# Kernel optimization log

Measured on AMD Instinct MI355X. Metric: run time of the kernel, lower is better.

## Reference

```python
import jax, jax.numpy as jnp
import numpy as np

T, N, G, H, COV, TW, E = 96, 1024, 128, 512, 8, 8, 32768
D2 = TW * (TW - 1)          # 56, GNN summary width
IN = COV + D2               # 64, exogenous input width


def setup_inputs() -> dict:
    key = jax.random.key(0)
    ks = jax.random.split(key, 32)
    s = 1.0 / np.sqrt(H)

    def u(k, shape):
        return jax.random.uniform(k, shape, jnp.float32, -s, s)

    inp = {
        "input": jax.random.normal(ks[0], (T, 1, IN), jnp.float32),
        "x_nodes": jax.random.normal(ks[1], (T, N, N), jnp.float32),
        "edge_index": jax.random.randint(ks[2], (T, 2, E), 0, N, dtype=jnp.int64),
        "W1": u(ks[3], (N, G)), "b1": u(ks[4], (G,)),
        "W2": u(ks[5], (G, G)), "b2": u(ks[6], (G,)),
        "Wfc": u(ks[7], (G * N, D2)), "bfc": u(ks[8], (D2,)),
        "W_ii": u(ks[9], (IN, H)), "W_gi": u(ks[10], (D2, H)), "W_hi": u(ks[11], (H, H)), "b_i": u(ks[12], (H,)),
        "W_if": u(ks[13], (IN, H)), "W_gf": u(ks[14], (D2, H)), "W_hf": u(ks[15], (H, H)), "b_f": u(ks[16], (H,)),
        "W_ig": u(ks[17], (IN, H)), "W_gg": u(ks[18], (D2, H)), "W_hg": u(ks[19], (H, H)), "b_g": u(ks[20], (H,)),
        "W_io": u(ks[21], (IN, H)), "W_go": u(ks[22], (D2, H)), "W_ho": u(ks[23], (H, H)), "b_o": u(ks[24], (H,)),
    }
    return inp


def reference(input, x_nodes, edge_index,
              W1, b1, W2, b2, Wfc, bfc,
              W_ii, W_gi, W_hi, b_i,
              W_if, W_gf, W_hf, b_f,
              W_ig, W_gg, W_hg, b_g,
              W_io, W_go, W_ho, b_o):
    self_loops = jnp.arange(N, dtype=edge_index.dtype)

    def gcn_conv(x, src, dst, dinv, W, b):
        # GCNConv: out[dst] += d^-1/2[src] d^-1/2[dst] * (x @ W)[src], plus bias
        xw = x @ W                                   # [N, F_out]
        norm = dinv[src] * dinv[dst]                 # [E+N]
        msg = xw[src] * norm[:, None]
        return jax.ops.segment_sum(msg, dst, num_segments=N) + b

    def step(carry, inputs):
        h, c = carry
        x_t, xg, ei = inputs                         # [1,IN], [N,N], [2,E]
        src = jnp.concatenate([ei[0], self_loops])   # add self-loops
        dst = jnp.concatenate([ei[1], self_loops])
        deg = jax.ops.segment_sum(jnp.ones(src.shape, jnp.float32), dst, num_segments=N)
        dinv = jnp.where(deg > 0, jax.lax.rsqrt(jnp.maximum(deg, 1.0)), 0.0)

        xh = jax.nn.relu(gcn_conv(xg, src, dst, dinv, W1, b1))
        xh = gcn_conv(xh, src, dst, dinv, W2, b2)    # [N, G]
        g = jax.nn.relu(xh.reshape(1, -1) @ Wfc + bfc)  # [1, D2]

        i = jax.nn.sigmoid(x_t @ W_ii + g @ W_gi + h @ W_hi + b_i)
        f = jax.nn.sigmoid(x_t @ W_if + g @ W_gf + h @ W_hf + b_f)
        gt = jnp.tanh(x_t @ W_ig + g @ W_gg + h @ W_hg + b_g)
        o = jax.nn.sigmoid(x_t @ W_io + g @ W_go + h @ W_ho + b_o)
        c = f * c + i * gt
        h = o * jnp.tanh(c)
        return (h, c), h

    h0 = jnp.zeros((1, H), jnp.float32)
    c0 = jnp.zeros((1, H), jnp.float32)
    (h, c), outputs = jax.lax.scan(step, (h0, c0), (input, x_nodes, edge_index))
    return outputs, h, c
```

## Files before the change

### kernel.cpp

```cpp
#include <hip/hip_runtime.h>
#include <stdint.h>

#define T_    96
#define TC_   32
#define N_    1024
#define G_    128
#define H_    512
#define E_    32768
#define EN_   33792
#define D2_   56
#define IN_   64
#define KFC_  131072

typedef __bf16 bf16_t;
typedef __bf16 bf16x8 __attribute__((ext_vector_type(8)));
typedef float  f32x4  __attribute__((ext_vector_type(4)));
typedef unsigned short u16;
typedef unsigned long long u64;

struct PtrQuadF { const float* p[4]; };

__device__ inline bf16x8 cvt8(const float* p) {
    const f32x4 a0 = *(const f32x4*)p;
    const f32x4 a1 = *(const f32x4*)(p + 4);
    bf16x8 r;
    r[0] = (bf16_t)a0[0]; r[1] = (bf16_t)a0[1]; r[2] = (bf16_t)a0[2]; r[3] = (bf16_t)a0[3];
    r[4] = (bf16_t)a1[0]; r[5] = (bf16_t)a1[1]; r[6] = (bf16_t)a1[2]; r[7] = (bf16_t)a1[3];
    return r;
}


__global__ __launch_bounds__(256) void deg_kernel(const int* __restrict__ ei, int* __restrict__ deg) {
    int t = blockIdx.y;
    int idx = blockIdx.x * 256 + threadIdx.x;
    if (idx >= EN_) return;
    int d = (idx < E_) ? ei[(size_t)t * 2 * E_ + E_ + idx] : (idx - E_);
    atomicAdd(&deg[t * N_ + d], 1);
}

__global__ __launch_bounds__(1024) void scan_kernel(const int* __restrict__ deg, int* __restrict__ rowptr,
                                                    int* __restrict__ fill, float* __restrict__ dinv) {
    int t = blockIdx.x, i = threadIdx.x;
    __shared__ int a[N_], b[N_];
    int d = deg[t * N_ + i];
    a[i] = d;
    __syncthreads();
    int* cur = a; int* nxt = b;
    for (int off = 1; off < N_; off <<= 1) {
        int v = cur[i];
        if (i >= off) v += cur[i - off];
        nxt[i] = v;
        __syncthreads();
        int* tmp = cur; cur = nxt; nxt = tmp;
    }
    int incl = cur[i];
    int start = incl - d + t * EN_;
    rowptr[t * N_ + i] = start;
    fill[t * N_ + i] = start;
    dinv[t * N_ + i] = rsqrtf((float)d);
}

__global__ __launch_bounds__(256) void fill_kernel(const int* __restrict__ ei, int* __restrict__ fill,
                                                   const float* __restrict__ dinv, u64* __restrict__ ecv) {
    int t = blockIdx.y;
    int idx = blockIdx.x * 256 + threadIdx.x;
    if (idx >= EN_) return;
    int s, d;
    if (idx < E_) {
        s = ei[(size_t)t * 2 * E_ + idx];
        d = ei[(size_t)t * 2 * E_ + E_ + idx];
    } else {
        s = d = idx - E_;
    }
    float nrm = dinv[t * N_ + s] * dinv[t * N_ + d];
    int pos = atomicAdd(&fill[t * N_ + d], 1);
    ecv[pos] = ((u64)__float_as_uint(nrm) << 32) | (unsigned int)s;
}


__global__ __launch_bounds__(256) void transpose_kernel(const float* __restrict__ src, bf16_t* __restrict__ dst,
                                                        int R, int C, int Cpad) {
    __shared__ bf16_t tile[64][65];
    int rb = blockIdx.x * 64, cb = blockIdx.y * 64;
    int tx = threadIdx.x & 63, ty = threadIdx.x >> 6;
#pragma unroll
    for (int i = 0; i < 16; i++) {
        int r = rb + ty * 16 + i;
        int c = cb + tx;
        float v = 0.f;
        if (r < R && c < C) v = src[(size_t)r * C + c];
        tile[ty * 16 + i][tx] = (bf16_t)v;
    }
    __syncthreads();
#pragma unroll
    for (int i = 0; i < 16; i++) {
        int c = cb + ty * 16 + i;
        int r = rb + tx;
        if (c < Cpad && r < R) dst[(size_t)c * R + r] = tile[tx][ty * 16 + i];
    }
}


__global__ __launch_bounds__(256) void transpose16_kernel(const bf16_t* __restrict__ src, bf16_t* __restrict__ dst) {
    __shared__ bf16_t tile[64][65];
    int tl = blockIdx.z;
    const bf16_t* s = src + (size_t)tl * 128 * N_;
    bf16_t* d = dst + (size_t)tl * N_ * 128;
    int rb = blockIdx.y * 64, cb = blockIdx.x * 64;
    int tx = threadIdx.x & 63, ty = threadIdx.x >> 6;
#pragma unroll
    for (int i = 0; i < 16; i++)
        tile[ty * 16 + i][tx] = s[(size_t)(rb + ty * 16 + i) * N_ + cb + tx];
    __syncthreads();
#pragma unroll
    for (int i = 0; i < 16; i++)
        d[(size_t)(cb + ty * 16 + i) * 128 + rb + tx] = tile[tx][ty * 16 + i];
}


__global__ __launch_bounds__(256) void whcvt_kernel(PtrQuadF Wh, bf16_t* __restrict__ dst) {
    int g = blockIdx.y;
    int idx = blockIdx.x * 256 + threadIdx.x;
    dst[(size_t)g * H_ * H_ + idx] = (bf16_t)Wh.p[g][idx];
}


template<bool BF32>
__global__ __launch_bounds__(256) void gemm_g(const bf16_t* __restrict__ A, const void* __restrict__ Bp,
                                              bf16_t* __restrict__ C, const float* __restrict__ bias, int relu,
                                              int K, int Mtiles, size_t sA, size_t sB, size_t sC, int ldc) {
    int t = blockIdx.y;
    int mi = blockIdx.x % Mtiles, ni = blockIdx.x / Mtiles;
    int tid = threadIdx.x;
    int w = tid >> 6, l = tid & 63;
    int wm = w & 1, wn = w >> 1;
    int lm = l & 15, lq = l >> 4;
    f32x4 acc[4][4] = {};
    const bf16_t* Ab = A + sA * t + (size_t)(mi * 128 + wm * 64 + lm) * K + lq * 8;
    size_t bO = sB * t + (size_t)(ni * 128 + wn * 64 + lm) * K + lq * 8;
    const bf16_t* Bb16 = (const bf16_t*)Bp + bO;
    const float*  Bb32 = (const float*)Bp + bO;
    for (int k0 = 0; k0 < K; k0 += 32) {
        bf16x8 af[4], bfv[4];
#pragma unroll
        for (int i = 0; i < 4; i++) af[i] = *(const bf16x8*)(Ab + (size_t)i * 16 * K + k0);
#pragma unroll
        for (int i = 0; i < 4; i++) {
            if (BF32) bfv[i] = cvt8(Bb32 + (size_t)i * 16 * K + k0);
            else      bfv[i] = *(const bf16x8*)(Bb16 + (size_t)i * 16 * K + k0);
        }
#pragma unroll
        for (int mt = 0; mt < 4; mt++)
#pragma unroll
            for (int nt = 0; nt < 4; nt++)
                acc[mt][nt] = __builtin_amdgcn_mfma_f32_16x16x32_bf16(af[mt], bfv[nt], acc[mt][nt], 0, 0, 0);
    }
#pragma unroll
    for (int mt = 0; mt < 4; mt++)
#pragma unroll
        for (int nt = 0; nt < 4; nt++) {
            int colg = ni * 128 + wn * 64 + nt * 16 + lm;
            float bv = bias ? bias[colg] : 0.f;
#pragma unroll
            for (int r = 0; r < 4; r++) {
                int row = mi * 128 + wm * 64 + mt * 16 + lq * 4 + r;
                float v = acc[mt][nt][r] + bv;
                if (relu) v = fmaxf(v, 0.f);
                C[sC * t + (size_t)row * ldc + colg] = (bf16_t)v;
            }
        }
}


__device__ inline void spmm_acc(u64 q, const bf16_t* Fb, int l, float& a0, float& a1) {
    int c = (int)(unsigned int)q;
    float wn = __uint_as_float((unsigned int)(q >> 32));
    unsigned int pk = *(const unsigned int*)(Fb + (size_t)c * 128 + 2 * l);
    a0 += wn * __uint_as_float(pk << 16);
    a1 += wn * __uint_as_float(pk & 0xffff0000u);
}

__global__ __launch_bounds__(256) void spmm_kernel(const int* __restrict__ rowptr, const int* __restrict__ deg,
                                                   const u64* __restrict__ ecv, const bf16_t* __restrict__ F,
                                                   const float* __restrict__ bias, int relu,
                                                   bf16_t* __restrict__ out, int t0) {
    int tl = blockIdx.y, t = t0 + tl;
    int w = threadIdx.x >> 6, l = threadIdx.x & 63;
    int r = blockIdx.x * 4 + w;
    int start = rowptr[t * N_ + r];
    int n = deg[t * N_ + r];
    const bf16_t* Fb = F + (size_t)tl * N_ * 128;
    const u64* ep = ecv + start;
    float a0 = 0.f, a1 = 0.f;
    int e = 0;
    for (; e + 4 <= n; e += 4) {
        u64 q0 = ep[e], q1 = ep[e + 1], q2 = ep[e + 2], q3 = ep[e + 3];
        spmm_acc(q0, Fb, l, a0, a1);
        spmm_acc(q1, Fb, l, a0, a1);
        spmm_acc(q2, Fb, l, a0, a1);
        spmm_acc(q3, Fb, l, a0, a1);
    }
    for (; e < n; e++) spmm_acc(ep[e], Fb, l, a0, a1);
    float v0 = a0 + bias[2 * l], v1 = a1 + bias[2 * l + 1];
    if (relu) { v0 = fmaxf(v0, 0.f); v1 = fmaxf(v1, 0.f); }
    bf16_t b0 = (bf16_t)v0, b1 = (bf16_t)v1;
    unsigned int po = (unsigned int)*(u16*)&b0 | ((unsigned int)*(u16*)&b1 << 16);
    *(unsigned int*)((u16*)(out + ((size_t)tl * N_ + r) * 128) + 2 * l) = po;
}


__global__ __launch_bounds__(256) void gfc_kernel(const bf16_t* __restrict__ XH2, const bf16_t* __restrict__ WfcT,
                                                  float* __restrict__ g_acc, int t0) {
    int tid = threadIdx.x;
    int w = tid >> 6, l = tid & 63;
    int lm = l & 15, lq = l >> 4;
    int n = w * 16 + lm;
    size_t k0 = (size_t)blockIdx.x * 1024;
    f32x4 acc[2] = {};
    const bf16_t* Ab = XH2 + (size_t)lm * KFC_ + k0 + lq * 8;
    const bf16_t* Bb = WfcT + (size_t)n * KFC_ + k0 + lq * 8;
    for (int ks = 0; ks < 32; ks++) {
        bf16x8 bfr = *(const bf16x8*)(Bb + ks * 32);
        bf16x8 a0  = *(const bf16x8*)(Ab + ks * 32);
        bf16x8 a1  = *(const bf16x8*)(Ab + (size_t)16 * KFC_ + ks * 32);
        acc[0] = __builtin_amdgcn_mfma_f32_16x16x32_bf16(a0, bfr, acc[0], 0, 0, 0);
        acc[1] = __builtin_amdgcn_mfma_f32_16x16x32_bf16(a1, bfr, acc[1], 0, 0, 0);
    }
#pragma unroll
    for (int mt = 0; mt < 2; mt++)
#pragma unroll
        for (int r = 0; r < 4; r++) {
            int t = t0 + mt * 16 + lq * 4 + r;
            if (n < D2_) atomicAdd(&g_acc[t * 64 + n], acc[mt][r]);
        }
}


__global__ __launch_bounds__(512) void pregate_kernel(const float* __restrict__ xin, const float* __restrict__ g_acc,
                                                      const float* __restrict__ bfc,
                                                      PtrQuadF Wi, PtrQuadF Wg, PtrQuadF Wb,
                                                      float* __restrict__ out) {
    int gate = blockIdx.x, t = blockIdx.y, j = threadIdx.x;
    __shared__ float gl[D2_];
    __shared__ float xl[IN_];
    if (j < D2_) gl[j] = fmaxf(g_acc[t * 64 + j] + bfc[j], 0.f);
    if (j < IN_) xl[j] = xin[t * IN_ + j];
    __syncthreads();
    const float* wi = Wi.p[gate];
    const float* wg = Wg.p[gate];
    float acc = Wb.p[gate][j];
#pragma unroll 4
    for (int k = 0; k < IN_; k++) acc += xl[k] * wi[k * H_ + j];
#pragma unroll 4
    for (int k = 0; k < D2_; k++) acc += gl[k] * wg[k * H_ + j];
    out[(t * 4 + gate) * H_ + j] = acc;
}


__global__ __launch_bounds__(256) void lstm_kernel(const bf16_t* __restrict__ Whb, const float* __restrict__ pregate,
                                                   u64* __restrict__ h_slot, float* __restrict__ out) {
    int tid = threadIdx.x, bid = blockIdx.x;
    int jl = tid >> 3, kc = tid & 7;
    int j = bid * 32 + jl;
    int k0 = kc * 64;

    uint32_t w[128];
#pragma unroll
    for (int g4 = 0; g4 < 4; g4++) {
        const bf16_t* W = Whb + (size_t)g4 * H_ * H_;
#pragma unroll
        for (int m = 0; m < 32; m++) {
            int k = k0 + 2 * m;
            uint32_t lo = *(const u16*)(W + (size_t)k * H_ + j);
            uint32_t hi = *(const u16*)(W + (size_t)(k + 1) * H_ + j);
            w[g4 * 32 + m] = lo | (hi << 16);
        }
    }

    __shared__ __align__(16) float hl[H_];
    hl[tid] = 0.f;
    hl[tid + 256] = 0.f;
    float c = 0.f;
    __syncthreads();

    for (int step = 0; step < 96; step++) {
        float p0 = 0.f, p1 = 0.f, p2 = 0.f, p3 = 0.f;
        if (kc == 0) {
            const float* pre = pregate + (size_t)step * (4 * H_);
            p0 = pre[0 * H_ + j]; p1 = pre[1 * H_ + j];
            p2 = pre[2 * H_ + j]; p3 = pre[3 * H_ + j];
        }

        float s0 = 0.f, s1 = 0.f, s2 = 0.f, s3 = 0.f;
        const float4* h4 = (const float4*)(hl + k0);
#pragma unroll
        for (int q = 0; q < 16; q++) {
            float4 hq = h4[q];
#pragma unroll
            for (int p = 0; p < 2; p++) {
                float h0 = p ? hq.z : hq.x;
                float h1 = p ? hq.w : hq.y;
                int mi = q * 2 + p;
                uint32_t wv;
                wv = w[0 * 32 + mi];
                s0 += __uint_as_float(wv << 16) * h0 + __uint_as_float(wv & 0xffff0000u) * h1;
                wv = w[1 * 32 + mi];
                s1 += __uint_as_float(wv << 16) * h0 + __uint_as_float(wv & 0xffff0000u) * h1;
                wv = w[2 * 32 + mi];
                s2 += __uint_as_float(wv << 16) * h0 + __uint_as_float(wv & 0xffff0000u) * h1;
                wv = w[3 * 32 + mi];
                s3 += __uint_as_float(wv << 16) * h0 + __uint_as_float(wv & 0xffff0000u) * h1;
            }
        }
        s0 += __shfl_xor(s0, 1); s0 += __shfl_xor(s0, 2); s0 += __shfl_xor(s0, 4);
        s1 += __shfl_xor(s1, 1); s1 += __shfl_xor(s1, 2); s1 += __shfl_xor(s1, 4);
        s2 += __shfl_xor(s2, 1); s2 += __shfl_xor(s2, 2); s2 += __shfl_xor(s2, 4);
        s3 += __shfl_xor(s3, 1); s3 += __shfl_xor(s3, 2); s3 += __shfl_xor(s3, 4);

        if (kc == 0) {
            float ig = 1.f / (1.f + __expf(-(s0 + p0)));
            float fg = 1.f / (1.f + __expf(-(s1 + p1)));
            float gg = tanhf(s2 + p2);
            float og = 1.f / (1.f + __expf(-(s3 + p3)));
            c = fg * c + ig * gg;
            float h = og * tanhf(c);
            if (step < 95) {
                u64 v = ((u64)(unsigned int)(step + 1) << 32) | (u64)__float_as_uint(h);
                __hip_atomic_store(&h_slot[(size_t)step * H_ + j], v, __ATOMIC_RELAXED, __HIP_MEMORY_SCOPE_AGENT);
            }
            out[step * H_ + j] = h;
            if (step == 95) {
                out[96 * H_ + j] = h;
                out[97 * H_ + j] = c;
            }
        }
        if (step < 95) {
            __syncthreads();
            if (tid < 64) {
                unsigned int want = (unsigned int)(step + 1);
                const u64* base = h_slot + (size_t)step * H_ + tid * 8;
                u64 v[8];
                int need = 0xff;
                while (need) {
#pragma unroll
                    for (int s = 0; s < 8; s++)
                        if (need & (1 << s))
                            v[s] = __hip_atomic_load(&base[s], __ATOMIC_RELAXED, __HIP_MEMORY_SCOPE_AGENT);
                    int nd = 0;
#pragma unroll
                    for (int s = 0; s < 8; s++)
                        if ((need & (1 << s)) && (unsigned int)(v[s] >> 32) != want) nd |= 1 << s;
                    need = nd;
                    if (need) __builtin_amdgcn_s_sleep(1);
                }
                float4 f0, f1;
                f0.x = __uint_as_float((unsigned int)v[0]); f0.y = __uint_as_float((unsigned int)v[1]);
                f0.z = __uint_as_float((unsigned int)v[2]); f0.w = __uint_as_float((unsigned int)v[3]);
                f1.x = __uint_as_float((unsigned int)v[4]); f1.y = __uint_as_float((unsigned int)v[5]);
                f1.z = __uint_as_float((unsigned int)v[6]); f1.w = __uint_as_float((unsigned int)v[7]);
                ((float4*)hl)[tid * 2] = f0;
                ((float4*)hl)[tid * 2 + 1] = f1;
            }
            __syncthreads();
        }
    }
}


extern "C" void kernel_launch(void* const* d_in, const int* in_sizes, int n_in,
                              void* d_out, int out_size, void* d_ws, size_t ws_size,
                              hipStream_t stream) {
    const float* xin    = (const float*)d_in[0];
    const float* xnodes = (const float*)d_in[1];
    const int*   ei     = (const int*)d_in[2];
    const float* W1  = (const float*)d_in[3];
    const float* b1  = (const float*)d_in[4];
    const float* W2  = (const float*)d_in[5];
    const float* b2  = (const float*)d_in[6];
    const float* Wfc = (const float*)d_in[7];
    const float* bfc = (const float*)d_in[8];

    PtrQuadF Wi = {{(const float*)d_in[9],  (const float*)d_in[13], (const float*)d_in[17], (const float*)d_in[21]}};
    PtrQuadF Wg = {{(const float*)d_in[10], (const float*)d_in[14], (const float*)d_in[18], (const float*)d_in[22]}};
    PtrQuadF Wh = {{(const float*)d_in[11], (const float*)d_in[15], (const float*)d_in[19], (const float*)d_in[23]}};
    PtrQuadF Wb = {{(const float*)d_in[12], (const float*)d_in[16], (const float*)d_in[20], (const float*)d_in[24]}};

    char* ws = (char*)d_ws;
    size_t off = 0;
    auto alloc = [&](size_t bytes) { void* p = ws + off; off += (bytes + 255) & ~(size_t)255; return p; };

    bf16_t* C1T     = (bf16_t*)alloc((size_t)TC_ * 128 * N_ * 2);
    bf16_t* C1      = (bf16_t*)alloc((size_t)TC_ * N_ * 128 * 2);
    bf16_t* XH1     = (bf16_t*)alloc((size_t)TC_ * N_ * 128 * 2);
    bf16_t* C2      = (bf16_t*)alloc((size_t)TC_ * N_ * 128 * 2);
    bf16_t* XH2     = (bf16_t*)alloc((size_t)TC_ * N_ * 128 * 2);
    u64*    ecv     = (u64*)   alloc((size_t)T_ * EN_ * 8);
    int*    deg     = (int*)   alloc((size_t)T_ * N_ * 4);
    int*    rowptr  = (int*)   alloc((size_t)T_ * N_ * 4);
    int*    fillp   = (int*)   alloc((size_t)T_ * N_ * 4);
    float*  dinv    = (float*) alloc((size_t)T_ * N_ * 4);
    bf16_t* W1t     = (bf16_t*)alloc((size_t)128 * 1024 * 2);
    bf16_t* W2t     = (bf16_t*)alloc((size_t)128 * 128 * 2);
    bf16_t* WfcT    = (bf16_t*)alloc((size_t)64 * KFC_ * 2);
    bf16_t* Whb     = (bf16_t*)alloc((size_t)4 * H_ * H_ * 2);
    float*  g_acc   = (float*) alloc((size_t)T_ * 64 * 4);
    float*  pregate = (float*) alloc((size_t)T_ * 4 * H_ * 4);
    u64*    h_slot  = (u64*)   alloc((size_t)T_ * H_ * 8);

    hipMemsetAsync(deg, 0, (size_t)T_ * N_ * 4, stream);
    hipMemsetAsync(g_acc, 0, (size_t)T_ * 64 * 4, stream);

    deg_kernel<<<dim3(132, T_), 256, 0, stream>>>(ei, deg);
    scan_kernel<<<T_, 1024, 0, stream>>>(deg, rowptr, fillp, dinv);
    fill_kernel<<<dim3(132, T_), 256, 0, stream>>>(ei, fillp, dinv, ecv);

    transpose_kernel<<<dim3(16, 2), 256, 0, stream>>>(W1, W1t, 1024, 128, 128);
    transpose_kernel<<<dim3(2, 2), 256, 0, stream>>>(W2, W2t, 128, 128, 128);
    transpose_kernel<<<dim3(2048, 1), 256, 0, stream>>>(Wfc, WfcT, KFC_, D2_, 64);
    whcvt_kernel<<<dim3(1024, 4), 256, 0, stream>>>(Wh, Whb);

    for (int c = 0; c < T_ / TC_; c++) {
        int t0 = c * TC_;
        gemm_g<true><<<dim3(8, TC_), 256, 0, stream>>>(
            W1t, xnodes + (size_t)t0 * N_ * N_, C1T, nullptr, 0,
            1024, 1, 0, (size_t)N_ * N_, (size_t)128 * N_, N_);
        transpose16_kernel<<<dim3(16, 2, TC_), 256, 0, stream>>>(C1T, C1);
        spmm_kernel<<<dim3(256, TC_), 256, 0, stream>>>(rowptr, deg, ecv, C1, b1, 1, XH1, t0);
        gemm_g<false><<<dim3(8, TC_), 256, 0, stream>>>(
            XH1, W2t, C2, nullptr, 0,
            128, 8, (size_t)N_ * 128, 0, (size_t)N_ * 128, 128);
        spmm_kernel<<<dim3(256, TC_), 256, 0, stream>>>(rowptr, deg, ecv, C2, b2, 0, XH2, t0);
        gfc_kernel<<<128, 256, 0, stream>>>(XH2, WfcT, g_acc, t0);
    }

    pregate_kernel<<<dim3(4, T_), 512, 0, stream>>>(xin, g_acc, bfc, Wi, Wg, Wb, pregate);

    lstm_kernel<<<16, 256, 0, stream>>>(Whb, pregate, h_slot, (float*)d_out);
}
```

Baseline: 1.587 ms.

## Fuse CSR build into one kernel, drop C1 transpose, enlarge time chunk

The degree, scan and fill kernels become one per-timestep block that does its degree counting and fill atomics in shared memory, which removes two launches, the memset and the global atomics. The first GCN GEMM now takes x_nodes as the fp32 A operand and writes C1 directly in node-major layout, so the intermediate transpose kernel and its buffer go away. The time chunk grows from 32 to 48 steps, and gfc handles three 16-row M tiles instead of two. In exchange, a single block per timestep builds the CSR serially over all edges, which limits parallelism, and the larger chunk needs bigger workspace buffers.

```diff
diff --git a/kernel.cpp b/kernel.cpp
--- a/kernel.cpp
+++ b/kernel.cpp
@@ -2,7 +2,7 @@
 #include <stdint.h>
 
 #define T_    96
-#define TC_   32
+#define TC_   48
 #define N_    1024
 #define G_    128
 #define H_    512
@@ -30,51 +30,45 @@
 }
 
 
-__global__ __launch_bounds__(256) void deg_kernel(const int* __restrict__ ei, int* __restrict__ deg) {
-    int t = blockIdx.y;
-    int idx = blockIdx.x * 256 + threadIdx.x;
-    if (idx >= EN_) return;
-    int d = (idx < E_) ? ei[(size_t)t * 2 * E_ + E_ + idx] : (idx - E_);
-    atomicAdd(&deg[t * N_ + d], 1);
-}
-
-__global__ __launch_bounds__(1024) void scan_kernel(const int* __restrict__ deg, int* __restrict__ rowptr,
-                                                    int* __restrict__ fill, float* __restrict__ dinv) {
-    int t = blockIdx.x, i = threadIdx.x;
-    __shared__ int a[N_], b[N_];
-    int d = deg[t * N_ + i];
-    a[i] = d;
-    __syncthreads();
-    int* cur = a; int* nxt = b;
+__global__ __launch_bounds__(1024) void build_kernel(const int* __restrict__ ei,
+                                                     int* __restrict__ rowptr_g, int* __restrict__ deg_g,
+                                                     u64* __restrict__ ecv) {
+    int t = blockIdx.x, tid = threadIdx.x;
+    __shared__ int sdeg[N_];
+    __shared__ int sa[N_], sb[N_];
+    __shared__ int sfill[N_];
+    __shared__ float sdinv[N_];
+    sdeg[tid] = 0;
+    __syncthreads();
+    const int* src_p = ei + (size_t)t * 2 * E_;
+    const int* dst_p = src_p + E_;
+    for (int e = tid; e < E_; e += 1024) atomicAdd(&sdeg[dst_p[e]], 1);
+    __syncthreads();
+    int d = sdeg[tid] + 1;
+    sa[tid] = d;
+    __syncthreads();
+    int* cur = sa; int* nxt = sb;
     for (int off = 1; off < N_; off <<= 1) {
-        int v = cur[i];
-        if (i >= off) v += cur[i - off];
-        nxt[i] = v;
+        int v = cur[tid];
+        if (tid >= off) v += cur[tid - off];
+        nxt[tid] = v;
         __syncthreads();
         int* tmp = cur; cur = nxt; nxt = tmp;
     }
-    int incl = cur[i];
-    int start = incl - d + t * EN_;
-    rowptr[t * N_ + i] = start;
-    fill[t * N_ + i] = start;
-    dinv[t * N_ + i] = rsqrtf((float)d);
-}
-
-__global__ __launch_bounds__(256) void fill_kernel(const int* __restrict__ ei, int* __restrict__ fill,
-                                                   const float* __restrict__ dinv, u64* __restrict__ ecv) {
-    int t = blockIdx.y;
-    int idx = blockIdx.x * 256 + threadIdx.x;
-    if (idx >= EN_) return;
-    int s, d;
-    if (idx < E_) {
-        s = ei[(size_t)t * 2 * E_ + idx];
-        d = ei[(size_t)t * 2 * E_ + E_ + idx];
-    } else {
-        s = d = idx - E_;
-    }
-    float nrm = dinv[t * N_ + s] * dinv[t * N_ + d];
-    int pos = atomicAdd(&fill[t * N_ + d], 1);
-    ecv[pos] = ((u64)__float_as_uint(nrm) << 32) | (unsigned int)s;
+    int start = cur[tid] - d + t * EN_;
+    rowptr_g[t * N_ + tid] = start;
+    deg_g[t * N_ + tid] = d;
+    sfill[tid] = start;
+    sdinv[tid] = rsqrtf((float)d);
+    __syncthreads();
+    for (int e = tid; e < EN_; e += 1024) {
+        int s, dd;
+        if (e < E_) { s = src_p[e]; dd = dst_p[e]; }
+        else        { s = dd = e - E_; }
+        float nrm = sdinv[s] * sdinv[dd];
+        int pos = atomicAdd(&sfill[dd], 1);
+        ecv[pos] = ((u64)__float_as_uint(nrm) << 32) | (unsigned int)s;
+    }
 }
 
 
@@ -101,23 +95,6 @@
 }
 
 
-__global__ __launch_bounds__(256) void transpose16_kernel(const bf16_t* __restrict__ src, bf16_t* __restrict__ dst) {
-    __shared__ bf16_t tile[64][65];
-    int tl = blockIdx.z;
-    const bf16_t* s = src + (size_t)tl * 128 * N_;
-    bf16_t* d = dst + (size_t)tl * N_ * 128;
-    int rb = blockIdx.y * 64, cb = blockIdx.x * 64;
-    int tx = threadIdx.x & 63, ty = threadIdx.x >> 6;
-#pragma unroll
-    for (int i = 0; i < 16; i++)
-        tile[ty * 16 + i][tx] = s[(size_t)(rb + ty * 16 + i) * N_ + cb + tx];
-    __syncthreads();
-#pragma unroll
-    for (int i = 0; i < 16; i++)
-        d[(size_t)(cb + ty * 16 + i) * 128 + rb + tx] = tile[tx][ty * 16 + i];
-}
-
-
 __global__ __launch_bounds__(256) void whcvt_kernel(PtrQuadF Wh, bf16_t* __restrict__ dst) {
     int g = blockIdx.y;
     int idx = blockIdx.x * 256 + threadIdx.x;
@@ -125,10 +102,10 @@
 }
 
 
-template<bool BF32>
-__global__ __launch_bounds__(256) void gemm_g(const bf16_t* __restrict__ A, const void* __restrict__ Bp,
+template<bool AF32>
+__global__ __launch_bounds__(256) void gemm_g(const void* __restrict__ Ap, const bf16_t* __restrict__ B,
                                               bf16_t* __restrict__ C, const float* __restrict__ bias, int relu,
-                                              int K, int Mtiles, size_t sA, size_t sB, size_t sC, int ldc) {
+                                              int K, int Mtiles, size_t sA, size_t sC, int ldc) {
     int t = blockIdx.y;
     int mi = blockIdx.x % Mtiles, ni = blockIdx.x / Mtiles;
     int tid = threadIdx.x;
@@ -136,19 +113,19 @@
     int wm = w & 1, wn = w >> 1;
     int lm = l & 15, lq = l >> 4;
     f32x4 acc[4][4] = {};
-    const bf16_t* Ab = A + sA * t + (size_t)(mi * 128 + wm * 64 + lm) * K + lq * 8;
-    size_t bO = sB * t + (size_t)(ni * 128 + wn * 64 + lm) * K + lq * 8;
-    const bf16_t* Bb16 = (const bf16_t*)Bp + bO;
-    const float*  Bb32 = (const float*)Bp + bO;
+    size_t aO = sA * t + (size_t)(mi * 128 + wm * 64 + lm) * K + lq * 8;
+    const bf16_t* Ab16 = (const bf16_t*)Ap + aO;
+    const float*  Ab32 = (const float*)Ap + aO;
+    const bf16_t* Bb = B + (size_t)(ni * 128 + wn * 64 + lm) * K + lq * 8;
     for (int k0 = 0; k0 < K; k0 += 32) {
         bf16x8 af[4], bfv[4];
 #pragma unroll
-        for (int i = 0; i < 4; i++) af[i] = *(const bf16x8*)(Ab + (size_t)i * 16 * K + k0);
-#pragma unroll
         for (int i = 0; i < 4; i++) {
-            if (BF32) bfv[i] = cvt8(Bb32 + (size_t)i * 16 * K + k0);
-            else      bfv[i] = *(const bf16x8*)(Bb16 + (size_t)i * 16 * K + k0);
-        }
+            if (AF32) af[i] = cvt8(Ab32 + (size_t)i * 16 * K + k0);
+            else      af[i] = *(const bf16x8*)(Ab16 + (size_t)i * 16 * K + k0);
+        }
+#pragma unroll
+        for (int i = 0; i < 4; i++) bfv[i] = *(const bf16x8*)(Bb + (size_t)i * 16 * K + k0);
 #pragma unroll
         for (int mt = 0; mt < 4; mt++)
 #pragma unroll
@@ -216,18 +193,19 @@
     int lm = l & 15, lq = l >> 4;
     int n = w * 16 + lm;
     size_t k0 = (size_t)blockIdx.x * 1024;
-    f32x4 acc[2] = {};
+    f32x4 acc[3] = {};
     const bf16_t* Ab = XH2 + (size_t)lm * KFC_ + k0 + lq * 8;
     const bf16_t* Bb = WfcT + (size_t)n * KFC_ + k0 + lq * 8;
     for (int ks = 0; ks < 32; ks++) {
         bf16x8 bfr = *(const bf16x8*)(Bb + ks * 32);
-        bf16x8 a0  = *(const bf16x8*)(Ab + ks * 32);
-        bf16x8 a1  = *(const bf16x8*)(Ab + (size_t)16 * KFC_ + ks * 32);
-        acc[0] = __builtin_amdgcn_mfma_f32_16x16x32_bf16(a0, bfr, acc[0], 0, 0, 0);
-        acc[1] = __builtin_amdgcn_mfma_f32_16x16x32_bf16(a1, bfr, acc[1], 0, 0, 0);
-    }
-#pragma unroll
-    for (int mt = 0; mt < 2; mt++)
+#pragma unroll
+        for (int mt = 0; mt < 3; mt++) {
+            bf16x8 a = *(const bf16x8*)(Ab + (size_t)(mt * 16) * KFC_ + ks * 32);
+            acc[mt] = __builtin_amdgcn_mfma_f32_16x16x32_bf16(a, bfr, acc[mt], 0, 0, 0);
+        }
+    }
+#pragma unroll
+    for (int mt = 0; mt < 3; mt++)
 #pragma unroll
         for (int r = 0; r < 4; r++) {
             int t = t0 + mt * 16 + lq * 4 + r;
@@ -389,7 +367,6 @@
     size_t off = 0;
     auto alloc = [&](size_t bytes) { void* p = ws + off; off += (bytes + 255) & ~(size_t)255; return p; };
 
-    bf16_t* C1T     = (bf16_t*)alloc((size_t)TC_ * 128 * N_ * 2);
     bf16_t* C1      = (bf16_t*)alloc((size_t)TC_ * N_ * 128 * 2);
     bf16_t* XH1     = (bf16_t*)alloc((size_t)TC_ * N_ * 128 * 2);
     bf16_t* C2      = (bf16_t*)alloc((size_t)TC_ * N_ * 128 * 2);
@@ -397,8 +374,6 @@
     u64*    ecv     = (u64*)   alloc((size_t)T_ * EN_ * 8);
     int*    deg     = (int*)   alloc((size_t)T_ * N_ * 4);
     int*    rowptr  = (int*)   alloc((size_t)T_ * N_ * 4);
-    int*    fillp   = (int*)   alloc((size_t)T_ * N_ * 4);
-    float*  dinv    = (float*) alloc((size_t)T_ * N_ * 4);
     bf16_t* W1t     = (bf16_t*)alloc((size_t)128 * 1024 * 2);
     bf16_t* W2t     = (bf16_t*)alloc((size_t)128 * 128 * 2);
     bf16_t* WfcT    = (bf16_t*)alloc((size_t)64 * KFC_ * 2);
@@ -407,12 +382,9 @@
     float*  pregate = (float*) alloc((size_t)T_ * 4 * H_ * 4);
     u64*    h_slot  = (u64*)   alloc((size_t)T_ * H_ * 8);
 
-    hipMemsetAsync(deg, 0, (size_t)T_ * N_ * 4, stream);
     hipMemsetAsync(g_acc, 0, (size_t)T_ * 64 * 4, stream);
 
-    deg_kernel<<<dim3(132, T_), 256, 0, stream>>>(ei, deg);
-    scan_kernel<<<T_, 1024, 0, stream>>>(deg, rowptr, fillp, dinv);
-    fill_kernel<<<dim3(132, T_), 256, 0, stream>>>(ei, fillp, dinv, ecv);
+    build_kernel<<<T_, 1024, 0, stream>>>(ei, rowptr, deg, ecv);
 
     transpose_kernel<<<dim3(16, 2), 256, 0, stream>>>(W1, W1t, 1024, 128, 128);
     transpose_kernel<<<dim3(2, 2), 256, 0, stream>>>(W2, W2t, 128, 128, 128);
@@ -422,13 +394,12 @@
     for (int c = 0; c < T_ / TC_; c++) {
         int t0 = c * TC_;
         gemm_g<true><<<dim3(8, TC_), 256, 0, stream>>>(
-            W1t, xnodes + (size_t)t0 * N_ * N_, C1T, nullptr, 0,
-            1024, 1, 0, (size_t)N_ * N_, (size_t)128 * N_, N_);
-        transpose16_kernel<<<dim3(16, 2, TC_), 256, 0, stream>>>(C1T, C1);
+            xnodes + (size_t)t0 * N_ * N_, W1t, C1, nullptr, 0,
+            1024, 8, (size_t)N_ * N_, (size_t)N_ * 128, 128);
         spmm_kernel<<<dim3(256, TC_), 256, 0, stream>>>(rowptr, deg, ecv, C1, b1, 1, XH1, t0);
         gemm_g<false><<<dim3(8, TC_), 256, 0, stream>>>(
             XH1, W2t, C2, nullptr, 0,
-            128, 8, (size_t)N_ * 128, 0, (size_t)N_ * 128, 128);
+            128, 8, (size_t)N_ * 128, (size_t)N_ * 128, 128);
         spmm_kernel<<<dim3(256, TC_), 256, 0, stream>>>(rowptr, deg, ecv, C2, b2, 0, XH2, t0);
         gfc_kernel<<<128, 256, 0, stream>>>(XH2, WfcT, g_acc, t0);
     }
```

After: 1.514 ms. 4.6% less time.
